# Kernel tuning notes

Measured on AMD Instinct MI355X. Metric: run time of the kernel, lower is better.

## Reference

```python
import jax, jax.numpy as jnp
import numpy as np

D_MODEL = 512
D_INNER = 1024   # 2 * d_model (Mamba default expand=2)
D_STATE = 16
D_CONV = 4
DT_RANK = 32     # ceil(d_model / 16)
N_LAYERS = 2
EPS = 1e-5


def rmsnorm(x, w):
    return x * jax.lax.rsqrt(jnp.mean(x * x, axis=-1, keepdims=True) + EPS) * w


def silu(x):
    return x * jax.nn.sigmoid(x)


def causal_conv1d(x, w, b):
    # x: [B,S,di], w: [di,d_conv] depthwise, b: [di]; causal left padding
    xt = jnp.transpose(x, (0, 2, 1))                 # [B,di,S]
    k = w[:, None, :]                                # [di,1,k]
    y = jax.lax.conv_general_dilated(
        xt, k, (1,), [(D_CONV - 1, 0)],
        dimension_numbers=('NCH', 'OIH', 'NCH'),
        feature_group_count=D_INNER)
    return jnp.transpose(y, (0, 2, 1)) + b


def selective_scan(u, dt, A, Bm, C, Dp):
    # u,dt: [B,S,di]; Bm,C: [B,S,ds]; A: [di,ds]; Dp: [di]
    def step(h, inp):
        dt_t, B_t, C_t, u_t = inp                    # [B,di],[B,ds],[B,ds],[B,di]
        dA = jnp.exp(dt_t[:, :, None] * A)           # [B,di,ds]
        h = dA * h + (dt_t * u_t)[:, :, None] * B_t[:, None, :]
        y = jnp.einsum('bds,bs->bd', h, C_t)
        return h, y

    B, S, di = u.shape
    h0 = jnp.zeros((B, di, D_STATE), u.dtype)
    xs = (jnp.swapaxes(dt, 0, 1), jnp.swapaxes(Bm, 0, 1),
          jnp.swapaxes(C, 0, 1), jnp.swapaxes(u, 0, 1))
    _, ys = jax.lax.scan(step, h0, xs)               # ys: [S,B,di]
    return jnp.swapaxes(ys, 0, 1) + u * Dp


def mamba_block(x, in_proj, conv_w, conv_b, xproj, dtproj, dtproj_b, A_log, Dp, outproj):
    xz = x @ in_proj.T                               # [B,S,2*di]
    u, z = jnp.split(xz, 2, axis=-1)
    u = silu(causal_conv1d(u, conv_w, conv_b))
    x_dbl = u @ xproj.T                              # [B,S,dt_rank+2*ds]
    dt = jax.nn.softplus(x_dbl[..., :DT_RANK] @ dtproj.T + dtproj_b)
    Bm = x_dbl[..., DT_RANK:DT_RANK + D_STATE]
    C = x_dbl[..., DT_RANK + D_STATE:]
    A = -jnp.exp(A_log)
    y = selective_scan(u, dt, A, Bm, C, Dp)
    return (y * silu(z)) @ outproj.T


def setup_inputs() -> dict:
    key = jax.random.key(0)
    ks = jax.random.split(key, 8)
    B, S, L = 2, 2048, N_LAYERS

    def w(k, shape, s=0.02):
        return jax.random.normal(k, shape, jnp.float32) * s

    inp = {}
    inp['input_data'] = jax.random.normal(ks[0], (B, D_MODEL, S), jnp.float32)
    inp['mask'] = jnp.ones((B, S), jnp.bool_)
    inp['in_proj_w'] = w(ks[1], (L, 2 * D_INNER, D_MODEL))
    inp['conv_w'] = w(ks[2], (L, D_INNER, D_CONV), 0.2)
    inp['conv_b'] = jnp.zeros((L, D_INNER), jnp.float32)
    inp['xproj_w'] = w(ks[3], (L, DT_RANK + 2 * D_STATE, D_INNER))
    inp['dtproj_w'] = w(ks[4], (L, D_INNER, DT_RANK), 0.1)
    inp['dtproj_b'] = w(ks[5], (L, D_INNER), 0.5) - 4.0  # softplus -> small dt
    inp['A_log'] = jnp.log(jnp.broadcast_to(
        jnp.arange(1, D_STATE + 1, dtype=jnp.float32), (L, D_INNER, D_STATE)))
    inp['Dp'] = jnp.ones((L, D_INNER), jnp.float32)
    inp['outproj_w'] = w(ks[6], (L, D_MODEL, D_INNER))
    inp['norm_w'] = jnp.ones((L, D_MODEL), jnp.float32)
    inp['final_norm_w'] = jnp.ones((D_MODEL,), jnp.float32)
    return inp


def reference(input_data, mask, in_proj_w, conv_w, conv_b, xproj_w, dtproj_w,
              dtproj_b, A_log, Dp, outproj_w, norm_w, final_norm_w):
    x = jnp.transpose(input_data, (0, 2, 1))         # [B,S,D]
    for l in range(N_LAYERS):
        x = x + mamba_block(rmsnorm(x, norm_w[l]), in_proj_w[l], conv_w[l],
                            conv_b[l], xproj_w[l], dtproj_w[l], dtproj_b[l],
                            A_log[l], Dp[l], outproj_w[l])
    tokens = rmsnorm(x, final_norm_w)                # [B,S,D] (lm_head=Identity)
    lengths = jnp.sum(mask.astype(jnp.int32), axis=1)
    idx = jnp.maximum(lengths - 1, 0)
    emb = jnp.take_along_axis(tokens, idx[:, None, None], axis=1)[:, 0]  # [B,D]
    return tokens, emb
```

## Files before the change

### kernel.cpp

```cpp
#include <hip/hip_runtime.h>
#include <hip/hip_bf16.h>
#include <cmath>

#define BQ 2
#define SQ 2048
#define DM 512
#define DI 1024
#define DSTATE 16
#define DCONV 4
#define DTR 32
#define NLAYERS 2
#define CHUNK 64
#define NCH (SQ / CHUNK)
#define LOG2E 1.4426950408889634f

typedef __attribute__((ext_vector_type(8))) short bf16x8;
typedef __attribute__((ext_vector_type(4))) float f32x4;

__device__ __forceinline__ unsigned short f2bf(float f) {
    __hip_bfloat16 h = __float2bfloat16(f);
    return *reinterpret_cast<unsigned short*>(&h);
}

__global__ __launch_bounds__(256) void k_transpose(const float* __restrict__ in,
                                                   float* __restrict__ out) {
    __shared__ float tile[32][33];
    int b = blockIdx.z;
    int s0 = blockIdx.x * 32, c0 = blockIdx.y * 32;
    int tx = threadIdx.x, ty = threadIdx.y;
#pragma unroll
    for (int i = 0; i < 4; i++)
        tile[ty + i * 8][tx] = in[((size_t)b * DM + c0 + ty + i * 8) * SQ + s0 + tx];
    __syncthreads();
#pragma unroll
    for (int i = 0; i < 4; i++)
        out[((size_t)b * SQ + s0 + ty + i * 8) * DM + c0 + tx] = tile[tx][ty + i * 8];
}

__global__ __launch_bounds__(256) void k_cvt(const float* __restrict__ in,
                                             unsigned short* __restrict__ out, int n4) {
    int i = blockIdx.x * 256 + threadIdx.x;
    if (i >= n4) return;
    float4 v = ((const float4*)in)[i];
    ushort4 o;
    o.x = f2bf(v.x); o.y = f2bf(v.y); o.z = f2bf(v.z); o.w = f2bf(v.w);
    ((ushort4*)out)[i] = o;
}

__global__ __launch_bounds__(256) void k_rmsnorm_bf(const float* __restrict__ x,
                                                    const float* __restrict__ w,
                                                    unsigned short* __restrict__ out) {
    int row = blockIdx.x;
    const float* xr = x + (size_t)row * DM;
    float v0 = xr[threadIdx.x];
    float v1 = xr[threadIdx.x + 256];
    float ss = v0 * v0 + v1 * v1;
#pragma unroll
    for (int off = 32; off >= 1; off >>= 1) ss += __shfl_xor(ss, off);
    __shared__ float wc[4];
    if ((threadIdx.x & 63) == 0) wc[threadIdx.x >> 6] = ss;
    __syncthreads();
    ss = wc[0] + wc[1] + wc[2] + wc[3];
    float r = rsqrtf(ss * (1.0f / DM) + 1e-5f);
    out[(size_t)row * DM + threadIdx.x] = f2bf(v0 * r * w[threadIdx.x]);
    out[(size_t)row * DM + threadIdx.x + 256] = f2bf(v1 * r * w[threadIdx.x + 256]);
}

__global__ __launch_bounds__(256) void k_rmsnorm_f32(const float* __restrict__ x,
                                                     const float* __restrict__ w,
                                                     float* __restrict__ out) {
    int row = blockIdx.x;
    const float* xr = x + (size_t)row * DM;
    float v0 = xr[threadIdx.x];
    float v1 = xr[threadIdx.x + 256];
    float ss = v0 * v0 + v1 * v1;
#pragma unroll
    for (int off = 32; off >= 1; off >>= 1) ss += __shfl_xor(ss, off);
    __shared__ float wc[4];
    if ((threadIdx.x & 63) == 0) wc[threadIdx.x >> 6] = ss;
    __syncthreads();
    ss = wc[0] + wc[1] + wc[2] + wc[3];
    float r = rsqrtf(ss * (1.0f / DM) + 1e-5f);
    out[(size_t)row * DM + threadIdx.x] = v0 * r * w[threadIdx.x];
    out[(size_t)row * DM + threadIdx.x + 256] = v1 * r * w[threadIdx.x + 256];
}

template<int BM, int BN, int AFR, int BFR>
__global__ __launch_bounds__(256) void k_gemm_bf16_t(const unsigned short* __restrict__ A, int lda,
                                                     const unsigned short* __restrict__ W, int ldw,
                                                     float* __restrict__ C, int ldc, int K,
                                                     const float* __restrict__ bias, int act,
                                                     const float* __restrict__ resid, int ldr) {
    __shared__ __align__(16) unsigned short As[BM * 32];
    __shared__ __align__(16) unsigned short Bs[BN * 32];
    const int bm = blockIdx.y * BM, bn = blockIdx.x * BN;
    const int tid = threadIdx.x;
    const int w = tid >> 6, l = tid & 63;
    const int wr = w >> 1, wc = w & 1;
    const int lg = l >> 4, lr16 = l & 15;
    f32x4 acc[AFR][BFR] = {};
    for (int k0 = 0; k0 < K; k0 += 32) {
        __syncthreads();
#pragma unroll
        for (int i = 0; i < BM / 64; i++) {
            int slot = i * 256 + tid;
            int row = slot >> 2, s = slot & 3;
            int sg = s ^ (row & 3);
            __builtin_amdgcn_global_load_lds(
                (const __attribute__((address_space(1))) unsigned int*)(A + (size_t)(bm + row) * lda + k0 + sg * 8),
                (__attribute__((address_space(3))) unsigned int*)(As + slot * 8), 16, 0, 0);
        }
#pragma unroll
        for (int i = 0; i < BN / 64; i++) {
            int slot = i * 256 + tid;
            int row = slot >> 2, s = slot & 3;
            int sg = s ^ (row & 3);
            __builtin_amdgcn_global_load_lds(
                (const __attribute__((address_space(1))) unsigned int*)(W + (size_t)(bn + row) * ldw + k0 + sg * 8),
                (__attribute__((address_space(3))) unsigned int*)(Bs + slot * 8), 16, 0, 0);
        }
        asm volatile("s_waitcnt vmcnt(0)" ::: "memory");
        __syncthreads();
        bf16x8 fa[AFR], fb[BFR];
#pragma unroll
        for (int f = 0; f < AFR; f++) {
            int ar = wr * (BM / 2) + f * 16 + lr16;
            fa[f] = *(const bf16x8*)&As[ar * 32 + (lg ^ (ar & 3)) * 8];
        }
#pragma unroll
        for (int f = 0; f < BFR; f++) {
            int br = wc * (BN / 2) + f * 16 + lr16;
            fb[f] = *(const bf16x8*)&Bs[br * 32 + (lg ^ (br & 3)) * 8];
        }
#pragma unroll
        for (int fi = 0; fi < AFR; fi++)
#pragma unroll
            for (int fj = 0; fj < BFR; fj++)
                acc[fi][fj] = __builtin_amdgcn_mfma_f32_16x16x32_bf16(fa[fi], fb[fj], acc[fi][fj], 0, 0, 0);
    }
#pragma unroll
    for (int fi = 0; fi < AFR; fi++)
#pragma unroll
        for (int fj = 0; fj < BFR; fj++)
#pragma unroll
            for (int r = 0; r < 4; r++) {
                int m = bm + wr * (BM / 2) + fi * 16 + lg * 4 + r;
                int n = bn + wc * (BN / 2) + fj * 16 + lr16;
                float v = acc[fi][fj][r];
                if (bias) v += bias[n];
                if (act == 1) v = fmaxf(v, 0.f) + log1pf(expf(-fabsf(v)));
                if (resid) v += resid[(size_t)m * ldr + n];
                C[(size_t)m * ldc + n] = v;
            }
}

__global__ __launch_bounds__(256) void k_gemm_n64_sk(const unsigned short* __restrict__ A, int lda,
                                                     const unsigned short* __restrict__ W, int ldw,
                                                     float* __restrict__ part) {
    __shared__ __align__(16) unsigned short As[128 * 32];
    __shared__ __align__(16) unsigned short Bs[64 * 32];
    const int bm = blockIdx.x * 128;
    const int koff = blockIdx.y * 128;
    const int tid = threadIdx.x;
    const int w = tid >> 6, l = tid & 63;
    const int lg = l >> 4, lr16 = l & 15;
    f32x4 acc[2][4] = {};
    for (int k0 = koff; k0 < koff + 128; k0 += 32) {
        __syncthreads();
#pragma unroll
        for (int i = 0; i < 2; i++) {
            int slot = i * 256 + tid;
            int row = slot >> 2, s = slot & 3;
            int sg = s ^ (row & 3);
            __builtin_amdgcn_global_load_lds(
                (const __attribute__((address_space(1))) unsigned int*)(A + (size_t)(bm + row) * lda + k0 + sg * 8),
                (__attribute__((address_space(3))) unsigned int*)(As + slot * 8), 16, 0, 0);
        }
        {
            int slot = tid;
            int row = slot >> 2, s = slot & 3;
            int sg = s ^ (row & 3);
            __builtin_amdgcn_global_load_lds(
                (const __attribute__((address_space(1))) unsigned int*)(W + (size_t)row * ldw + k0 + sg * 8),
                (__attribute__((address_space(3))) unsigned int*)(Bs + slot * 8), 16, 0, 0);
        }
        asm volatile("s_waitcnt vmcnt(0)" ::: "memory");
        __syncthreads();
        bf16x8 fa[2], fb[4];
#pragma unroll
        for (int f = 0; f < 2; f++) {
            int ar = w * 32 + f * 16 + lr16;
            fa[f] = *(const bf16x8*)&As[ar * 32 + (lg ^ (ar & 3)) * 8];
        }
#pragma unroll
        for (int f = 0; f < 4; f++) {
            int br = f * 16 + lr16;
            fb[f] = *(const bf16x8*)&Bs[br * 32 + (lg ^ (br & 3)) * 8];
        }
#pragma unroll
        for (int fi = 0; fi < 2; fi++)
#pragma unroll
            for (int fj = 0; fj < 4; fj++)
                acc[fi][fj] = __builtin_amdgcn_mfma_f32_16x16x32_bf16(fa[fi], fb[fj], acc[fi][fj], 0, 0, 0);
    }
    float* out = part + (size_t)blockIdx.y * ((size_t)BQ * SQ * 64);
#pragma unroll
    for (int fi = 0; fi < 2; fi++)
#pragma unroll
        for (int fj = 0; fj < 4; fj++)
#pragma unroll
            for (int r = 0; r < 4; r++) {
                int m = bm + w * 32 + fi * 16 + lg * 4 + r;
                int n = fj * 16 + lr16;
                out[(size_t)m * 64 + n] = acc[fi][fj][r];
            }
}

__global__ __launch_bounds__(256) void k_xdbl_reduce(const float* __restrict__ part,
                                                     float* __restrict__ xdbl,
                                                     unsigned short* __restrict__ xbf) {
    const int n4 = BQ * SQ * 64 / 4;
    int i = blockIdx.x * 256 + threadIdx.x;
    if (i >= n4) return;
    float4 s = ((const float4*)part)[i];
#pragma unroll
    for (int ks = 1; ks < 8; ks++) {
        float4 t = ((const float4*)part)[(size_t)ks * n4 + i];
        s.x += t.x; s.y += t.y; s.z += t.z; s.w += t.w;
    }
    ((float4*)xdbl)[i] = s;
    ushort4 o;
    o.x = f2bf(s.x); o.y = f2bf(s.y); o.z = f2bf(s.z); o.w = f2bf(s.w);
    ((ushort4*)xbf)[i] = o;
}

__global__ __launch_bounds__(256) void k_conv_silu(const float* __restrict__ xz,
                                                   const float* __restrict__ cw,
                                                   const float* __restrict__ cb,
                                                   float* __restrict__ u,
                                                   unsigned short* __restrict__ ubf) {
    int b = blockIdx.z;
    int t0 = blockIdx.x * 64;
    int d = blockIdx.y * 256 + threadIdx.x;
    float4 wv = ((const float4*)cw)[d];
    float bias = cb[d];
    const size_t rs = 2 * DI;
    size_t base = (size_t)b * SQ * rs + d;
    float x0 = 0.f, x1 = 0.f, x2 = 0.f;
    if (t0 > 0) {
        x0 = xz[base + (size_t)(t0 - 3) * rs];
        x1 = xz[base + (size_t)(t0 - 2) * rs];
        x2 = xz[base + (size_t)(t0 - 1) * rs];
    }
    for (int t = t0; t < t0 + 64; t++) {
        float x3 = xz[base + (size_t)t * rs];
        float a = bias + wv.x * x0 + wv.y * x1 + wv.z * x2 + wv.w * x3;
        float sig = 1.f / (1.f + __expf(-a));
        float v = a * sig;
        size_t o = (size_t)(b * SQ + t) * DI + d;
        u[o] = v;
        ubf[o] = f2bf(v);
        x0 = x1; x1 = x2; x2 = x3;
    }
}

__global__ __launch_bounds__(256) void k_scan_p1(const float* __restrict__ xdbl,
                                                 const float* __restrict__ dt,
                                                 const float* __restrict__ u,
                                                 const float* __restrict__ A_log,
                                                 float* __restrict__ hend,
                                                 float* __restrict__ dchunk) {
    int bc = blockIdx.x >> 4;
    int d0 = (blockIdx.x & 15) << 6;
    int b = bc >> 5;
    int c = bc & (NCH - 1);
    int tid = threadIdx.x;
    int q = tid & 3, dl = tid >> 2;
    int d = d0 + dl;
    float4 av = *(const float4*)&A_log[((size_t)d << 4) + 4 * q];
    float a0 = -expf(av.x) * LOG2E, a1 = -expf(av.y) * LOG2E;
    float a2 = -expf(av.z) * LOG2E, a3 = -expf(av.w) * LOG2E;
    float h0 = 0.f, h1 = 0.f, h2 = 0.f, h3 = 0.f, sumdt = 0.f;
    __shared__ __align__(16) float sdt[32][68], su[32][68];
    __shared__ __align__(16) float sB[32][20];
    int tbase = c * CHUNK;
    for (int t0 = 0; t0 < CHUNK; t0 += 32) {
        __syncthreads();
#pragma unroll
        for (int i = 0; i < 2; i++) {
            int e = i * 256 + tid;
            int tt = e >> 4, j4 = e & 15;
            size_t rowm = (size_t)(b * SQ + tbase + t0 + tt);
            *(float4*)&sdt[tt][j4 * 4] = *(const float4*)&dt[rowm * DI + d0 + j4 * 4];
            *(float4*)&su[tt][j4 * 4]  = *(const float4*)&u[rowm * DI + d0 + j4 * 4];
        }
        if (tid < 128) {
            int tt = tid >> 2, j4 = tid & 3;
            size_t rowm = (size_t)(b * SQ + tbase + t0 + tt);
            *(float4*)&sB[tt][j4 * 4] = *(const float4*)&xdbl[rowm * 64 + DTR + j4 * 4];
        }
        __syncthreads();
        for (int tt = 0; tt < 32; tt++) {
            float dtv = sdt[tt][dl], uv = su[tt][dl];
            float dtu = dtv * uv;
            sumdt += dtv;
            float4 Bv = *(const float4*)&sB[tt][4 * q];
            h0 = exp2f(dtv * a0) * h0 + dtu * Bv.x;
            h1 = exp2f(dtv * a1) * h1 + dtu * Bv.y;
            h2 = exp2f(dtv * a2) * h2 + dtu * Bv.z;
            h3 = exp2f(dtv * a3) * h3 + dtu * Bv.w;
        }
    }
    size_t o = ((size_t)bc << 14) + ((size_t)d << 4) + 4 * q;
    *(float4*)&hend[o] = make_float4(h0, h1, h2, h3);
    *(float4*)&dchunk[o] = make_float4(exp2f(a0 * sumdt), exp2f(a1 * sumdt),
                                       exp2f(a2 * sumdt), exp2f(a3 * sumdt));
}

__global__ __launch_bounds__(256) void k_scan_p2(const float* __restrict__ hend,
                                                 const float* __restrict__ dchunk,
                                                 float* __restrict__ hstart) {
    int tid = blockIdx.x * 256 + threadIdx.x;
    int b = tid >> 14;
    int ds = tid & 16383;
    float h = 0.f;
#pragma unroll
    for (int c = 0; c < NCH; c++) {
        size_t o = (((size_t)(b * NCH + c)) << 14) + ds;
        hstart[o] = h;
        h = dchunk[o] * h + hend[o];
    }
}

__global__ __launch_bounds__(256) void k_scan_p3(const float* __restrict__ xdbl,
                                                 const float* __restrict__ dt,
                                                 const float* __restrict__ u,
                                                 const float* __restrict__ xz,
                                                 const float* __restrict__ A_log,
                                                 const float* __restrict__ Dp,
                                                 const float* __restrict__ hstart,
                                                 unsigned short* __restrict__ yout) {
    int bc = blockIdx.x >> 4;
    int d0 = (blockIdx.x & 15) << 6;
    int b = bc >> 5;
    int c = bc & (NCH - 1);
    int tid = threadIdx.x;
    int q = tid & 3, dl = tid >> 2;
    int d = d0 + dl;
    float4 av = *(const float4*)&A_log[((size_t)d << 4) + 4 * q];
    float a0 = -expf(av.x) * LOG2E, a1 = -expf(av.y) * LOG2E;
    float a2 = -expf(av.z) * LOG2E, a3 = -expf(av.w) * LOG2E;
    size_t o = ((size_t)bc << 14) + ((size_t)d << 4) + 4 * q;
    float4 hv = *(const float4*)&hstart[o];
    float h0 = hv.x, h1 = hv.y, h2 = hv.z, h3 = hv.w;
    float Dv = Dp[d];
    __shared__ __align__(16) float sdt[32][68], su[32][68], sz[32][68];
    __shared__ __align__(16) float sBC[32][36];
    int tbase = c * CHUNK;
    for (int t0 = 0; t0 < CHUNK; t0 += 32) {
        __syncthreads();
#pragma unroll
        for (int i = 0; i < 2; i++) {
            int e = i * 256 + tid;
            int tt = e >> 4, j4 = e & 15;
            size_t rowm = (size_t)(b * SQ + tbase + t0 + tt);
            *(float4*)&sdt[tt][j4 * 4] = *(const float4*)&dt[rowm * DI + d0 + j4 * 4];
            *(float4*)&su[tt][j4 * 4]  = *(const float4*)&u[rowm * DI + d0 + j4 * 4];
            *(float4*)&sz[tt][j4 * 4]  = *(const float4*)&xz[rowm * (2 * DI) + DI + d0 + j4 * 4];
        }
        {
            int tt = tid >> 3, j4 = tid & 7;
            size_t rowm = (size_t)(b * SQ + tbase + t0 + tt);
            *(float4*)&sBC[tt][j4 * 4] = *(const float4*)&xdbl[rowm * 64 + DTR + j4 * 4];
        }
        __syncthreads();
        for (int tt = 0; tt < 32; tt++) {
            float dtv = sdt[tt][dl], uv = su[tt][dl];
            float dtu = dtv * uv;
            float4 Bv = *(const float4*)&sBC[tt][4 * q];
            float4 Cv = *(const float4*)&sBC[tt][16 + 4 * q];
            h0 = exp2f(dtv * a0) * h0 + dtu * Bv.x;
            h1 = exp2f(dtv * a1) * h1 + dtu * Bv.y;
            h2 = exp2f(dtv * a2) * h2 + dtu * Bv.z;
            h3 = exp2f(dtv * a3) * h3 + dtu * Bv.w;
            float y = h0 * Cv.x + h1 * Cv.y + h2 * Cv.z + h3 * Cv.w;
            y += __shfl_xor(y, 1);
            y += __shfl_xor(y, 2);
            if (q == 0) {
                y += uv * Dv;
                float zv = sz[tt][dl];
                float g = zv / (1.f + __expf(-zv));
                yout[(size_t)(b * SQ + tbase + t0 + tt) * DI + d] = f2bf(y * g);
            }
        }
    }
}

__global__ __launch_bounds__(256) void k_emb(const float* __restrict__ tokens,
                                             const int* __restrict__ mask,
                                             float* __restrict__ emb) {
    int b = blockIdx.x;
    int cnt = 0;
    for (int i = threadIdx.x; i < SQ; i += 256) cnt += mask[b * SQ + i] ? 1 : 0;
#pragma unroll
    for (int off = 32; off >= 1; off >>= 1) cnt += __shfl_xor(cnt, off);
    __shared__ int wc[4];
    if ((threadIdx.x & 63) == 0) wc[threadIdx.x >> 6] = cnt;
    __syncthreads();
    int total = wc[0] + wc[1] + wc[2] + wc[3];
    int idx = total > 0 ? total - 1 : 0;
    for (int i = threadIdx.x; i < DM; i += 256)
        emb[b * DM + i] = tokens[((size_t)b * SQ + idx) * DM + i];
}

extern "C" void kernel_launch(void* const* d_in, const int* in_sizes, int n_in,
                              void* d_out, int out_size, void* d_ws, size_t ws_size,
                              hipStream_t stream) {
    const float* input_data   = (const float*)d_in[0];
    const int*   mask         = (const int*)d_in[1];
    const float* in_proj_w    = (const float*)d_in[2];
    const float* conv_w       = (const float*)d_in[3];
    const float* conv_b       = (const float*)d_in[4];
    const float* xproj_w      = (const float*)d_in[5];
    const float* dtproj_w     = (const float*)d_in[6];
    const float* dtproj_b     = (const float*)d_in[7];
    const float* A_log        = (const float*)d_in[8];
    const float* Dp           = (const float*)d_in[9];
    const float* outproj_w    = (const float*)d_in[10];
    const float* norm_w       = (const float*)d_in[11];
    const float* final_norm_w = (const float*)d_in[12];
    float* out = (float*)d_out;

    const size_t M = (size_t)BQ * SQ;
    const size_t CS = (size_t)BQ * NCH * DI * DSTATE;
    float* x              = (float*)d_ws;
    unsigned short* xn_bf = (unsigned short*)(x + M * DM);
    float* xz             = (float*)(xn_bf + M * DM);
    float* u              = xz + M * 2 * DI;
    float* xdbl           = u + M * DI;
    float* dtb            = xdbl + M * 64;
    unsigned short* ubf   = (unsigned short*)(dtb + M * DI);
    unsigned short* ybf   = ubf + M * DI;
    float* hend           = (float*)(ybf + M * DI);
    float* dchunk         = hend + CS;
    float* hstart         = dchunk + CS;
    float* xpart          = hstart + CS;
    unsigned short* xdbl_bf = (unsigned short*)(xpart + 8 * M * 64);
    unsigned short* wbf_in  = xdbl_bf + M * 64;
    unsigned short* wbf_out = wbf_in + (size_t)NLAYERS * 2 * DI * DM;
    unsigned short* wbf_x   = wbf_out + (size_t)NLAYERS * DM * DI;
    unsigned short* wbf_dt  = wbf_x + (size_t)NLAYERS * 64 * DI;

    {
        int n4 = NLAYERS * 2 * DI * DM / 4;
        k_cvt<<<(n4 + 255) / 256, 256, 0, stream>>>(in_proj_w, wbf_in, n4);
        n4 = NLAYERS * DM * DI / 4;
        k_cvt<<<(n4 + 255) / 256, 256, 0, stream>>>(outproj_w, wbf_out, n4);
        n4 = NLAYERS * 64 * DI / 4;
        k_cvt<<<(n4 + 255) / 256, 256, 0, stream>>>(xproj_w, wbf_x, n4);
        n4 = NLAYERS * DI * DTR / 4;
        k_cvt<<<(n4 + 255) / 256, 256, 0, stream>>>(dtproj_w, wbf_dt, n4);
    }

    k_transpose<<<dim3(SQ / 32, DM / 32, BQ), dim3(32, 8), 0, stream>>>(input_data, x);

    for (int l = 0; l < NLAYERS; l++) {
        k_rmsnorm_bf<<<M, 256, 0, stream>>>(x, norm_w + (size_t)l * DM, xn_bf);
        k_gemm_bf16_t<128, 128, 4, 4><<<dim3(2 * DI / 128, M / 128), 256, 0, stream>>>(
            xn_bf, DM, wbf_in + (size_t)l * 2 * DI * DM, DM, xz, 2 * DI, DM,
            nullptr, 0, nullptr, 0);
        k_conv_silu<<<dim3(SQ / 64, DI / 256, BQ), 256, 0, stream>>>(
            xz, conv_w + (size_t)l * DI * DCONV, conv_b + (size_t)l * DI, u, ubf);
        k_gemm_n64_sk<<<dim3(M / 128, 8), 256, 0, stream>>>(
            ubf, DI, wbf_x + (size_t)l * 64 * DI, DI, xpart);
        k_xdbl_reduce<<<(BQ * SQ * 64 / 4 + 255) / 256, 256, 0, stream>>>(
            xpart, xdbl, xdbl_bf);
        k_gemm_bf16_t<64, 128, 2, 4><<<dim3(DI / 128, M / 64), 256, 0, stream>>>(
            xdbl_bf, 64, wbf_dt + (size_t)l * DI * DTR, DTR, dtb, DI, DTR,
            dtproj_b + (size_t)l * DI, 1, nullptr, 0);
        k_scan_p1<<<BQ * NCH * (DI / 64), 256, 0, stream>>>(
            xdbl, dtb, u, A_log + (size_t)l * DI * DSTATE, hend, dchunk);
        k_scan_p2<<<(BQ * DI * DSTATE) / 256, 256, 0, stream>>>(hend, dchunk, hstart);
        k_scan_p3<<<BQ * NCH * (DI / 64), 256, 0, stream>>>(
            xdbl, dtb, u, xz, A_log + (size_t)l * DI * DSTATE, Dp + (size_t)l * DI,
            hstart, ybf);
        k_gemm_bf16_t<64, 128, 2, 4><<<dim3(DM / 128, M / 64), 256, 0, stream>>>(
            ybf, DI, wbf_out + (size_t)l * DM * DI, DI, x, DM, DI,
            nullptr, 0, x, DM);
    }

    k_rmsnorm_f32<<<M, 256, 0, stream>>>(x, final_norm_w, out);
    k_emb<<<BQ, 256, 0, stream>>>(out, mask, out + M * DM);
}
```

Baseline: 473.7 us.

## Halve scan chunk size, prefetch z gates into registers, fuse weight conversions

```diff
diff --git a/kernel.cpp b/kernel.cpp
--- a/kernel.cpp
+++ b/kernel.cpp
@@ -10,7 +10,7 @@
 #define DCONV 4
 #define DTR 32
 #define NLAYERS 2
-#define CHUNK 64
+#define CHUNK 32
 #define NCH (SQ / CHUNK)
 #define LOG2E 1.4426950408889634f
 
@@ -37,14 +37,31 @@
         out[((size_t)b * SQ + s0 + ty + i * 8) * DM + c0 + tx] = tile[tx][ty + i * 8];
 }
 
-__global__ __launch_bounds__(256) void k_cvt(const float* __restrict__ in,
-                                             unsigned short* __restrict__ out, int n4) {
+#define N4_IN  (NLAYERS * 2 * DI * DM / 4)
+#define N4_OUT (NLAYERS * DM * DI / 4)
+#define N4_X   (NLAYERS * 64 * DI / 4)
+#define N4_DT  (NLAYERS * DI * DTR / 4)
+#define N4_ALL (N4_IN + N4_OUT + N4_X + N4_DT)
+
+__global__ __launch_bounds__(256) void k_cvt_all(const float* __restrict__ s0,
+                                                 const float* __restrict__ s1,
+                                                 const float* __restrict__ s2,
+                                                 const float* __restrict__ s3,
+                                                 unsigned short* __restrict__ d0,
+                                                 unsigned short* __restrict__ d1,
+                                                 unsigned short* __restrict__ d2,
+                                                 unsigned short* __restrict__ d3) {
     int i = blockIdx.x * 256 + threadIdx.x;
-    if (i >= n4) return;
-    float4 v = ((const float4*)in)[i];
+    if (i >= N4_ALL) return;
+    const float* src; unsigned short* dst; int j = i;
+    if (j < N4_IN) { src = s0; dst = d0; }
+    else if ((j -= N4_IN) < N4_OUT) { src = s1; dst = d1; }
+    else if ((j -= N4_OUT) < N4_X) { src = s2; dst = d2; }
+    else { j -= N4_X; src = s3; dst = d3; }
+    float4 v = ((const float4*)src)[j];
     ushort4 o;
     o.x = f2bf(v.x); o.y = f2bf(v.y); o.z = f2bf(v.z); o.w = f2bf(v.w);
-    ((ushort4*)out)[i] = o;
+    ((ushort4*)dst)[j] = o;
 }
 
 __global__ __launch_bounds__(256) void k_rmsnorm_bf(const float* __restrict__ x,
@@ -272,7 +289,7 @@
                                                  float* __restrict__ dchunk) {
     int bc = blockIdx.x >> 4;
     int d0 = (blockIdx.x & 15) << 6;
-    int b = bc >> 5;
+    int b = bc >> 6;
     int c = bc & (NCH - 1);
     int tid = threadIdx.x;
     int q = tid & 3, dl = tid >> 2;
@@ -284,32 +301,30 @@
     __shared__ __align__(16) float sdt[32][68], su[32][68];
     __shared__ __align__(16) float sB[32][20];
     int tbase = c * CHUNK;
-    for (int t0 = 0; t0 < CHUNK; t0 += 32) {
-        __syncthreads();
-#pragma unroll
-        for (int i = 0; i < 2; i++) {
-            int e = i * 256 + tid;
-            int tt = e >> 4, j4 = e & 15;
-            size_t rowm = (size_t)(b * SQ + tbase + t0 + tt);
-            *(float4*)&sdt[tt][j4 * 4] = *(const float4*)&dt[rowm * DI + d0 + j4 * 4];
-            *(float4*)&su[tt][j4 * 4]  = *(const float4*)&u[rowm * DI + d0 + j4 * 4];
-        }
-        if (tid < 128) {
-            int tt = tid >> 2, j4 = tid & 3;
-            size_t rowm = (size_t)(b * SQ + tbase + t0 + tt);
-            *(float4*)&sB[tt][j4 * 4] = *(const float4*)&xdbl[rowm * 64 + DTR + j4 * 4];
-        }
-        __syncthreads();
-        for (int tt = 0; tt < 32; tt++) {
-            float dtv = sdt[tt][dl], uv = su[tt][dl];
-            float dtu = dtv * uv;
-            sumdt += dtv;
-            float4 Bv = *(const float4*)&sB[tt][4 * q];
-            h0 = exp2f(dtv * a0) * h0 + dtu * Bv.x;
-            h1 = exp2f(dtv * a1) * h1 + dtu * Bv.y;
-            h2 = exp2f(dtv * a2) * h2 + dtu * Bv.z;
-            h3 = exp2f(dtv * a3) * h3 + dtu * Bv.w;
-        }
+#pragma unroll
+    for (int i = 0; i < 2; i++) {
+        int e = i * 256 + tid;
+        int tt = e >> 4, j4 = e & 15;
+        size_t rowm = (size_t)(b * SQ + tbase + tt);
+        *(float4*)&sdt[tt][j4 * 4] = *(const float4*)&dt[rowm * DI + d0 + j4 * 4];
+        *(float4*)&su[tt][j4 * 4]  = *(const float4*)&u[rowm * DI + d0 + j4 * 4];
+    }
+    if (tid < 128) {
+        int tt = tid >> 2, j4 = tid & 3;
+        size_t rowm = (size_t)(b * SQ + tbase + tt);
+        *(float4*)&sB[tt][j4 * 4] = *(const float4*)&xdbl[rowm * 64 + DTR + j4 * 4];
+    }
+    __syncthreads();
+#pragma unroll
+    for (int tt = 0; tt < 32; tt++) {
+        float dtv = sdt[tt][dl], uv = su[tt][dl];
+        float dtu = dtv * uv;
+        sumdt += dtv;
+        float4 Bv = *(const float4*)&sB[tt][4 * q];
+        h0 = exp2f(dtv * a0) * h0 + dtu * Bv.x;
+        h1 = exp2f(dtv * a1) * h1 + dtu * Bv.y;
+        h2 = exp2f(dtv * a2) * h2 + dtu * Bv.z;
+        h3 = exp2f(dtv * a3) * h3 + dtu * Bv.w;
     }
     size_t o = ((size_t)bc << 14) + ((size_t)d << 4) + 4 * q;
     *(float4*)&hend[o] = make_float4(h0, h1, h2, h3);
@@ -324,7 +339,6 @@
     int b = tid >> 14;
     int ds = tid & 16383;
     float h = 0.f;
-#pragma unroll
     for (int c = 0; c < NCH; c++) {
         size_t o = (((size_t)(b * NCH + c)) << 14) + ds;
         hstart[o] = h;
@@ -342,11 +356,18 @@
                                                  unsigned short* __restrict__ yout) {
     int bc = blockIdx.x >> 4;
     int d0 = (blockIdx.x & 15) << 6;
-    int b = bc >> 5;
+    int b = bc >> 6;
     int c = bc & (NCH - 1);
     int tid = threadIdx.x;
     int q = tid & 3, dl = tid >> 2;
     int d = d0 + dl;
+    int tbase = c * CHUNK;
+    float zr[8];
+#pragma unroll
+    for (int i = 0; i < 8; i++) {
+        size_t rowm = (size_t)(b * SQ + tbase + i * 4 + q);
+        zr[i] = xz[rowm * (2 * DI) + DI + d];
+    }
     float4 av = *(const float4*)&A_log[((size_t)d << 4) + 4 * q];
     float a0 = -expf(av.x) * LOG2E, a1 = -expf(av.y) * LOG2E;
     float a2 = -expf(av.z) * LOG2E, a3 = -expf(av.w) * LOG2E;
@@ -354,44 +375,40 @@
     float4 hv = *(const float4*)&hstart[o];
     float h0 = hv.x, h1 = hv.y, h2 = hv.z, h3 = hv.w;
     float Dv = Dp[d];
-    __shared__ __align__(16) float sdt[32][68], su[32][68], sz[32][68];
+    __shared__ __align__(16) float sdt[32][68], su[32][68];
     __shared__ __align__(16) float sBC[32][36];
-    int tbase = c * CHUNK;
-    for (int t0 = 0; t0 < CHUNK; t0 += 32) {
-        __syncthreads();
-#pragma unroll
-        for (int i = 0; i < 2; i++) {
-            int e = i * 256 + tid;
-            int tt = e >> 4, j4 = e & 15;
-            size_t rowm = (size_t)(b * SQ + tbase + t0 + tt);
-            *(float4*)&sdt[tt][j4 * 4] = *(const float4*)&dt[rowm * DI + d0 + j4 * 4];
-            *(float4*)&su[tt][j4 * 4]  = *(const float4*)&u[rowm * DI + d0 + j4 * 4];
-            *(float4*)&sz[tt][j4 * 4]  = *(const float4*)&xz[rowm * (2 * DI) + DI + d0 + j4 * 4];
-        }
-        {
-            int tt = tid >> 3, j4 = tid & 7;
-            size_t rowm = (size_t)(b * SQ + tbase + t0 + tt);
-            *(float4*)&sBC[tt][j4 * 4] = *(const float4*)&xdbl[rowm * 64 + DTR + j4 * 4];
-        }
-        __syncthreads();
-        for (int tt = 0; tt < 32; tt++) {
-            float dtv = sdt[tt][dl], uv = su[tt][dl];
-            float dtu = dtv * uv;
-            float4 Bv = *(const float4*)&sBC[tt][4 * q];
-            float4 Cv = *(const float4*)&sBC[tt][16 + 4 * q];
-            h0 = exp2f(dtv * a0) * h0 + dtu * Bv.x;
-            h1 = exp2f(dtv * a1) * h1 + dtu * Bv.y;
-            h2 = exp2f(dtv * a2) * h2 + dtu * Bv.z;
-            h3 = exp2f(dtv * a3) * h3 + dtu * Bv.w;
-            float y = h0 * Cv.x + h1 * Cv.y + h2 * Cv.z + h3 * Cv.w;
-            y += __shfl_xor(y, 1);
-            y += __shfl_xor(y, 2);
-            if (q == 0) {
-                y += uv * Dv;
-                float zv = sz[tt][dl];
-                float g = zv / (1.f + __expf(-zv));
-                yout[(size_t)(b * SQ + tbase + t0 + tt) * DI + d] = f2bf(y * g);
-            }
+#pragma unroll
+    for (int i = 0; i < 2; i++) {
+        int e = i * 256 + tid;
+        int tt = e >> 4, j4 = e & 15;
+        size_t rowm = (size_t)(b * SQ + tbase + tt);
+        *(float4*)&sdt[tt][j4 * 4] = *(const float4*)&dt[rowm * DI + d0 + j4 * 4];
+        *(float4*)&su[tt][j4 * 4]  = *(const float4*)&u[rowm * DI + d0 + j4 * 4];
+    }
+    {
+        int tt = tid >> 3, j4 = tid & 7;
+        size_t rowm = (size_t)(b * SQ + tbase + tt);
+        *(float4*)&sBC[tt][j4 * 4] = *(const float4*)&xdbl[rowm * 64 + DTR + j4 * 4];
+    }
+    __syncthreads();
+#pragma unroll
+    for (int tt = 0; tt < 32; tt++) {
+        float dtv = sdt[tt][dl], uv = su[tt][dl];
+        float dtu = dtv * uv;
+        float4 Bv = *(const float4*)&sBC[tt][4 * q];
+        float4 Cv = *(const float4*)&sBC[tt][16 + 4 * q];
+        h0 = exp2f(dtv * a0) * h0 + dtu * Bv.x;
+        h1 = exp2f(dtv * a1) * h1 + dtu * Bv.y;
+        h2 = exp2f(dtv * a2) * h2 + dtu * Bv.z;
+        h3 = exp2f(dtv * a3) * h3 + dtu * Bv.w;
+        float y = h0 * Cv.x + h1 * Cv.y + h2 * Cv.z + h3 * Cv.w;
+        y += __shfl_xor(y, 1);
+        y += __shfl_xor(y, 2);
+        if (q == (tt & 3)) {
+            y += uv * Dv;
+            float zv = zr[tt >> 2];
+            float g = zv / (1.f + __expf(-zv));
+            yout[(size_t)(b * SQ + tbase + tt) * DI + d] = f2bf(y * g);
         }
     }
 }
@@ -451,16 +468,8 @@
     unsigned short* wbf_x   = wbf_out + (size_t)NLAYERS * DM * DI;
     unsigned short* wbf_dt  = wbf_x + (size_t)NLAYERS * 64 * DI;
 
-    {
-        int n4 = NLAYERS * 2 * DI * DM / 4;
-        k_cvt<<<(n4 + 255) / 256, 256, 0, stream>>>(in_proj_w, wbf_in, n4);
-        n4 = NLAYERS * DM * DI / 4;
-        k_cvt<<<(n4 + 255) / 256, 256, 0, stream>>>(outproj_w, wbf_out, n4);
-        n4 = NLAYERS * 64 * DI / 4;
-        k_cvt<<<(n4 + 255) / 256, 256, 0, stream>>>(xproj_w, wbf_x, n4);
-        n4 = NLAYERS * DI * DTR / 4;
-        k_cvt<<<(n4 + 255) / 256, 256, 0, stream>>>(dtproj_w, wbf_dt, n4);
-    }
+    k_cvt_all<<<(N4_ALL + 255) / 256, 256, 0, stream>>>(
+        in_proj_w, outproj_w, xproj_w, dtproj_w, wbf_in, wbf_out, wbf_x, wbf_dt);
 
     k_transpose<<<dim3(SQ / 32, DM / 32, BQ), dim3(32, 8), 0, stream>>>(input_data, x);
 
```

After: 469.0 us. Within noise of the previous version (-1.0%).
